# Kernel tuning notes

Hardware: AMD Instinct MI355X
Metric: run time of the kernel (lower is better)

Reference implementation:

```python
import jax, jax.numpy as jnp
import numpy as np

B, N = 32, 512            # batch, max nodes per graph
F_DIM, M_DIM = 1024, 256  # node feature dim, first hidden dim
N_SEM = 8                 # number of semantic-class experts
XYZ, DIM_E = 3, 8
OUT_SIZE = 2 * XYZ + DIM_E  # 14 (default reg branch)
EPS = 1e-8                # padding value used by out_seq_to_batch


def setup_inputs() -> dict:
    key = jax.random.key(0)
    ks = jax.random.split(key, 12)
    def w(k, shape, fan_in):
        return jax.random.normal(k, shape, jnp.float32) / np.float32(np.sqrt(fan_in))
    return {
        "nodes": jax.random.normal(ks[0], (B, N, F_DIM), jnp.float32),
        "sem": jax.random.randint(ks[1], (B, N), 0, N_SEM, jnp.int32),
        "lengths": jax.random.randint(ks[2], (B,), 64, N + 1, jnp.int32),
        # y expert MLPs (4 layers), stacked over experts
        "W1": w(ks[3], (N_SEM, F_DIM, M_DIM), F_DIM), "b1": jnp.zeros((N_SEM, M_DIM), jnp.float32),
        "W2": w(ks[4], (N_SEM, M_DIM, 64), M_DIM),   "b2": jnp.zeros((N_SEM, 64), jnp.float32),
        "W3": w(ks[5], (N_SEM, 64, 32), 64),         "b3": jnp.zeros((N_SEM, 32), jnp.float32),
        "W4": w(ks[6], (N_SEM, 32, OUT_SIZE), 32),   "b4": jnp.zeros((N_SEM, OUT_SIZE), jnp.float32),
        # rot expert MLPs (2 layers), stacked over experts
        "R1": w(ks[7], (N_SEM, F_DIM, M_DIM), F_DIM), "rb1": jnp.zeros((N_SEM, M_DIM), jnp.float32),
        "R2": w(ks[8], (N_SEM, M_DIM, XYZ), M_DIM),   "rb2": jnp.zeros((N_SEM, XYZ), jnp.float32),
    }


def _prim_mlps(nodes, sem, lengths, W1, b1, W2, b2, W3, b3, W4, b4, R1, rb1, R2, rb2):
    Bn, Nn, Fd = nodes.shape
    x = nodes.reshape(-1, Fd)                       # [T, F], T = B*N tokens
    semf = sem.reshape(-1)                          # [T] expert id per token
    # dense dispatch: run every expert on all tokens, then select per token
    h1 = jax.nn.relu(jnp.einsum('tf,efm->etm', x, W1) + b1[:, None, :])   # [E,T,M]
    h2 = jax.nn.relu(jnp.einsum('etm,emh->eth', h1, W2) + b2[:, None, :]) # [E,T,64]
    h3 = jax.nn.relu(jnp.einsum('eth,ehg->etg', h2, W3) + b3[:, None, :]) # [E,T,32]
    y_all = jnp.einsum('etg,ego->eto', h3, W4) + b4[:, None, :]           # [E,T,OUT]
    r1 = jax.nn.relu(jnp.einsum('tf,efm->etm', x, R1) + rb1[:, None, :])  # [E,T,M]
    rot_all = jnp.einsum('etm,emo->eto', r1, R2) + rb2[:, None, :]        # [E,T,XYZ]
    t = jnp.arange(x.shape[0])
    y = y_all[semf, t]                              # [T, OUT]
    rot = rot_all[semf, t]                          # [T, XYZ]
    out = jnp.concatenate([y, rot], axis=-1).reshape(Bn, Nn, -1)
    # positions beyond each graph's length are filled with eps (out_seq_to_batch)
    mask = (jnp.arange(Nn)[None, :] < lengths[:, None])[:, :, None]
    return jnp.where(mask, out, jnp.float32(EPS))


def reference(nodes, sem, lengths, W1, b1, W2, b2, W3, b3, W4, b4, R1, rb1, R2, rb2):
    return _prim_mlps(nodes, sem, lengths, W1, b1, W2, b2, W3, b3, W4, b4,
                      R1, rb1, R2, rb2)
```

## Files before the change

kernel.cpp:

```cpp
#include <hip/hip_runtime.h>
#include <stdint.h>

#define T_TOK 16384
#define NE 8
#define EPSV 1e-8f
#define MAXC128 136
#define MAXC64  264

#define WS_PERM   0
#define WS_PART   65536
#define WS_OFFS   67584
#define WS_WT     131072
#define WS_H1     (WS_WT + 8*512*1024*2)
#define WS_W2T    (WS_H1 + 16448*512*2)
#define WS_W3T    (WS_W2T + 8*64*256*2)
#define WS_W4T    (WS_W3T + 8*32*64*2)
#define WS_R2T    (WS_W4T + 8*16*32*2)

typedef __attribute__((ext_vector_type(8))) short bf16x8;
typedef __attribute__((ext_vector_type(4))) float f32x4;

__device__ __forceinline__ unsigned short f2bf(float f) {
    unsigned u = __float_as_uint(f);
    u += 0x7fffu + ((u >> 16) & 1u);
    return (unsigned short)(u >> 16);
}

__device__ __forceinline__ void gl_lds16(const void* g, void* l) {
    __builtin_amdgcn_global_load_lds(
        (const __attribute__((address_space(1))) void*)g,
        (__attribute__((address_space(3))) void*)l,
        16, 0, 0);
}

__device__ __forceinline__ bool chunk_lookup(const int* __restrict__ offs, int c, int csize,
                                             int& e, int& base, int& len) {
    int acc = 0;
#pragma unroll
    for (int i = 0; i < NE; i++) {
        int s = offs[i], t = offs[i + 1];
        int cc = (t - s + csize - 1) / csize;
        if (c < acc + cc) {
            e = i;
            base = s + (c - acc) * csize;
            len = (t - base < csize) ? (t - base) : csize;
            return true;
        }
        acc += cc;
    }
    return false;
}

__global__ __launch_bounds__(256) void k_prep1(const float* __restrict__ W1,
                                               const float* __restrict__ R1,
                                               const float* __restrict__ W2,
                                               const float* __restrict__ W3,
                                               const float* __restrict__ W4,
                                               const float* __restrict__ R2,
                                               const int* __restrict__ sem,
                                               unsigned short* __restrict__ wt,
                                               unsigned short* __restrict__ w2t,
                                               unsigned short* __restrict__ w3t,
                                               unsigned short* __restrict__ w4t,
                                               unsigned short* __restrict__ r2t,
                                               int* __restrict__ ws_i) {
    __shared__ float tile[64][65];
    int id = blockIdx.x, tid = threadIdx.x;
    if (id >= 1024) {
        __shared__ int cnt[NE];
        int hb = id - 1024, lane = tid & 63;
        if (tid < NE) cnt[tid] = 0;
        __syncthreads();
        int s = sem[hb * 256 + tid];
#pragma unroll
        for (int e = 0; e < NE; e++) {
            unsigned long long m = __ballot(s == e);
            if (lane == e) atomicAdd(&cnt[e], (int)__popcll(m));
        }
        __syncthreads();
        if (tid < NE) ws_i[(WS_PART >> 2) + hb * NE + tid] = cnt[tid];
        return;
    }
    int e = id >> 7, rem = id & 127;
    int ny = rem >> 4, kx = rem & 15;
    int k0 = kx * 64, n0 = ny * 64;
    const float* src = (n0 < 256) ? (W1 + (size_t)e * 1024 * 256 + n0)
                                  : (R1 + (size_t)e * 1024 * 256 + (n0 - 256));
    int rr = tid >> 4;
    int cg = (tid & 15) * 4;
#pragma unroll
    for (int p = 0; p < 4; p++) {
        int kk = p * 16 + rr;
        float4 v = *(const float4*)(src + (size_t)(k0 + kk) * 256 + cg);
        tile[kk][cg] = v.x; tile[kk][cg + 1] = v.y; tile[kk][cg + 2] = v.z; tile[kk][cg + 3] = v.w;
    }
    __syncthreads();
    int nn = tid >> 3;
    int k8 = tid & 7;
#pragma unroll
    for (int p = 0; p < 2; p++) {
        int n = p * 32 + nn;
        unsigned w[4];
#pragma unroll
        for (int j = 0; j < 4; j++) {
            float f0 = tile[k8 * 8 + 2 * j][n];
            float f1 = tile[k8 * 8 + 2 * j + 1][n];
            w[j] = (unsigned)f2bf(f0) | ((unsigned)f2bf(f1) << 16);
        }
        *(uint4*)(wt + (size_t)(e * 512 + n0 + n) * 1024 + k0 + k8 * 8) =
            make_uint4(w[0], w[1], w[2], w[3]);
    }
    if (ny == 0) {
        int x = kx;
        for (int j = tid; j < 1024; j += 256) {
            int idx = x * 1024 + j; int k = idx & 255, n = idx >> 8;
            w2t[(size_t)(e * 64 + n) * 256 + k] = f2bf(W2[(size_t)e * 16384 + k * 64 + n]);
        }
        if (tid < 128) {
            int idx = x * 128 + tid; int k = idx & 63, n = idx >> 6;
            w3t[(size_t)(e * 32 + n) * 64 + k] = f2bf(W3[(size_t)e * 2048 + k * 32 + n]);
        }
        if (tid < 32) {
            int idx = x * 32 + tid; int k = idx & 31, n = idx >> 5;
            w4t[(size_t)(e * 16 + n) * 32 + k] = (n < 14) ? f2bf(W4[(size_t)e * 448 + k * 14 + n])
                                                          : (unsigned short)0;
        }
        {
            int idx = x * 256 + tid; int k = idx & 255, n = idx >> 8;
            r2t[(size_t)(e * 16 + n) * 256 + k] = (n < 3) ? f2bf(R2[(size_t)e * 768 + k * 3 + n])
                                                          : (unsigned short)0;
        }
    }
}

__global__ __launch_bounds__(256) void k_scatter(const int* __restrict__ sem, int* __restrict__ ws_i) {
    __shared__ int parts[64 * NE];
    __shared__ int tot[NE], preb[NE], ebase[NE + 1];
    __shared__ int cur[NE];
    int b = blockIdx.x, tid = threadIdx.x, lane = tid & 63;
    parts[tid] = ws_i[(WS_PART >> 2) + tid];
    parts[256 + tid] = ws_i[(WS_PART >> 2) + 256 + tid];
    __syncthreads();
    if (tid < NE) {
        int t = 0, p = 0;
        for (int bb = 0; bb < 64; bb++) {
            int v = parts[bb * NE + tid];
            t += v;
            if (bb < b) p += v;
        }
        tot[tid] = t; preb[tid] = p;
    }
    __syncthreads();
    if (tid == 0) {
        int base = 0;
        for (int e = 0; e < NE; e++) { ebase[e] = base; base += tot[e]; }
        ebase[NE] = base;
        if (b == 0)
            for (int e = 0; e <= NE; e++) ws_i[(WS_OFFS >> 2) + e] = ebase[e];
    }
    __syncthreads();
    if (tid < NE) cur[tid] = ebase[tid] + preb[tid];
    __syncthreads();
    int i = b * 256 + tid;
    int s = sem[i];
    int* perm = ws_i + (WS_PERM >> 2);
#pragma unroll
    for (int e = 0; e < NE; e++) {
        unsigned long long m = __ballot(s == e);
        if (s == e) {
            int leader = (int)__builtin_ctzll(m);
            int rank = (int)__popcll(m & ((1ull << lane) - 1ull));
            int bpos = 0;
            if (lane == leader) bpos = atomicAdd(&cur[e], (int)__popcll(m));
            bpos = __shfl(bpos, leader, 64);
            perm[bpos + rank] = i;
        }
    }
}

__global__ __launch_bounds__(256) void k_gemm(const float* __restrict__ nodes,
                                              const unsigned short* __restrict__ wt,
                                              const float* __restrict__ b1,
                                              const float* __restrict__ rb1,
                                              const int* __restrict__ ws_i,
                                              unsigned short* __restrict__ h1) {
    __shared__ __align__(16) short As[128 * 64];
    __shared__ __align__(16) short Bs[128 * 64];
    int e, base, len;
    if (!chunk_lookup(ws_i + (WS_OFFS >> 2), blockIdx.x, 128, e, base, len)) return;
    int n0 = blockIdx.y * 128;
    int tid = threadIdx.x;
    int wave = tid >> 6, lane = tid & 63;
    int quad = lane >> 4, lr = lane & 15;
    int wm = (wave & 1) * 64, wn = (wave >> 1) * 64;
    const int* perm = ws_i + (WS_PERM >> 2);

    f32x4 acc[4][4];
#pragma unroll
    for (int i = 0; i < 4; i++)
#pragma unroll
        for (int j = 0; j < 4; j++) acc[i][j] = (f32x4){0.f, 0.f, 0.f, 0.f};

    const unsigned short* Bg = wt + (size_t)(e * 512 + n0) * 1024;

    int cs = (tid & 7) ^ ((tid >> 3) & 7);
    const float* srcA[4];
    const unsigned short* srcB[4];
    int dstA[4], dstB[4];
#pragma unroll
    for (int i = 0; i < 4; i++) {
        int R = i * 32 + (tid >> 3);
        int row = base + R; if (row > T_TOK - 1) row = T_TOK - 1;
        srcA[i] = nodes + (size_t)perm[row] * 1024 + cs * 8;
        dstA[i] = (i * 256 + tid) * 8;
        int s = i * 256 + wave * 64 + lane;
        int r = s >> 3, cb = (s & 7) ^ (r & 7);
        srcB[i] = Bg + (size_t)r * 1024 + cb * 8;
        dstB[i] = (i * 256 + wave * 64) * 8;
    }

    for (int kb = 0; kb < 16; kb++) {
        __syncthreads();
#pragma unroll
        for (int i = 0; i < 4; i++)
            gl_lds16(srcB[i] + kb * 64, Bs + dstB[i]);
#pragma unroll
        for (int i = 0; i < 4; i++) {
            const float4* p = (const float4*)(srcA[i] + kb * 64);
            float4 a = p[0], b = p[1];
            unsigned r0 = (unsigned)f2bf(a.x) | ((unsigned)f2bf(a.y) << 16);
            unsigned r1 = (unsigned)f2bf(a.z) | ((unsigned)f2bf(a.w) << 16);
            unsigned r2 = (unsigned)f2bf(b.x) | ((unsigned)f2bf(b.y) << 16);
            unsigned r3 = (unsigned)f2bf(b.z) | ((unsigned)f2bf(b.w) << 16);
            *(uint4*)(As + dstA[i]) = make_uint4(r0, r1, r2, r3);
        }
        __syncthreads();

        bf16x8 af[2][4], bfr[2][4];
#pragma unroll
        for (int im = 0; im < 4; im++) {
            int r = wm + im * 16 + lr;
#pragma unroll
            for (int kh = 0; kh < 2; kh++) {
                int q = kh * 4 + quad;
                af[kh][im] = *(const bf16x8*)(As + (r * 8 + (q ^ (r & 7))) * 8);
            }
        }
#pragma unroll
        for (int in = 0; in < 4; in++) {
            int r = wn + in * 16 + lr;
#pragma unroll
            for (int kh = 0; kh < 2; kh++) {
                int q = kh * 4 + quad;
                bfr[kh][in] = *(const bf16x8*)(Bs + (r * 8 + (q ^ (r & 7))) * 8);
            }
        }
#pragma unroll
        for (int kh = 0; kh < 2; kh++)
#pragma unroll
            for (int im = 0; im < 4; im++)
#pragma unroll
                for (int in = 0; in < 4; in++)
                    acc[im][in] = __builtin_amdgcn_mfma_f32_16x16x32_bf16(af[kh][im], bfr[kh][in], acc[im][in], 0, 0, 0);
    }

#pragma unroll
    for (int in = 0; in < 4; in++) {
        int gcol = n0 + wn + in * 16 + lr;
        float bias = (gcol < 256) ? b1[e * 256 + gcol] : rb1[e * 256 + gcol - 256];
#pragma unroll
        for (int im = 0; im < 4; im++) {
#pragma unroll
            for (int v = 0; v < 4; v++) {
                int r = wm + im * 16 + quad * 4 + v;
                if (r < len) {
                    float val = fmaxf(acc[im][in][v] + bias, 0.f);
                    h1[(size_t)(base + r) * 512 + gcol] = f2bf(val);
                }
            }
        }
    }
}

__global__ __launch_bounds__(256) void k_tail(const unsigned short* __restrict__ h1,
                                              const int* __restrict__ ws_i,
                                              const unsigned short* __restrict__ w2t,
                                              const unsigned short* __restrict__ w3t,
                                              const unsigned short* __restrict__ w4t,
                                              const unsigned short* __restrict__ r2t,
                                              const float* __restrict__ b2,
                                              const float* __restrict__ b3,
                                              const float* __restrict__ b4,
                                              const float* __restrict__ rb2,
                                              const int* __restrict__ lengths,
                                              float* __restrict__ out) {
    __shared__ __align__(16) unsigned short h2s[4][16][64];
    __shared__ __align__(16) unsigned short h3s[4][16][32];

    int e, base, len;
    if (!chunk_lookup(ws_i + (WS_OFFS >> 2), blockIdx.x, 64, e, base, len)) return;
    int tid = threadIdx.x, wave = tid >> 6, lane = tid & 63;
    int quad = lane >> 4, lr = lane & 15;
    int m0 = wave * 16;

    const unsigned short* Ap = h1 + (size_t)(base + m0) * 512;

    f32x4 acc2[4];
#pragma unroll
    for (int t = 0; t < 4; t++) {
        float bb = b2[e * 64 + t * 16 + lr];
        acc2[t] = (f32x4){bb, bb, bb, bb};
    }
    f32x4 accr;
    { float bb = (lr < 3) ? rb2[e * 3 + lr] : 0.f; accr = (f32x4){bb, bb, bb, bb}; }

    const unsigned short* W2e = w2t + (size_t)e * 64 * 256;
    const unsigned short* R2e = r2t + (size_t)e * 16 * 256;
#pragma unroll
    for (int kk = 0; kk < 8; kk++) {
        int k0 = kk * 32;
        bf16x8 a = *(const bf16x8*)(Ap + lr * 512 + k0 + quad * 8);
#pragma unroll
        for (int t = 0; t < 4; t++) {
            bf16x8 b = *(const bf16x8*)(W2e + (t * 16 + lr) * 256 + k0 + quad * 8);
            acc2[t] = __builtin_amdgcn_mfma_f32_16x16x32_bf16(a, b, acc2[t], 0, 0, 0);
        }
        bf16x8 ar = *(const bf16x8*)(Ap + lr * 512 + 256 + k0 + quad * 8);
        bf16x8 br = *(const bf16x8*)(R2e + lr * 256 + k0 + quad * 8);
        accr = __builtin_amdgcn_mfma_f32_16x16x32_bf16(ar, br, accr, 0, 0, 0);
    }
#pragma unroll
    for (int t = 0; t < 4; t++)
#pragma unroll
        for (int v = 0; v < 4; v++)
            h2s[wave][quad * 4 + v][t * 16 + lr] = f2bf(fmaxf(acc2[t][v], 0.f));

    f32x4 acc3[2];
#pragma unroll
    for (int t = 0; t < 2; t++) {
        float bb = b3[e * 32 + t * 16 + lr];
        acc3[t] = (f32x4){bb, bb, bb, bb};
    }
    const unsigned short* W3e = w3t + (size_t)e * 32 * 64;
#pragma unroll
    for (int kk = 0; kk < 2; kk++) {
        int k0 = kk * 32;
        bf16x8 a = *(const bf16x8*)(&h2s[wave][lr][k0 + quad * 8]);
#pragma unroll
        for (int t = 0; t < 2; t++) {
            bf16x8 b = *(const bf16x8*)(W3e + (t * 16 + lr) * 64 + k0 + quad * 8);
            acc3[t] = __builtin_amdgcn_mfma_f32_16x16x32_bf16(a, b, acc3[t], 0, 0, 0);
        }
    }
#pragma unroll
    for (int t = 0; t < 2; t++)
#pragma unroll
        for (int v = 0; v < 4; v++)
            h3s[wave][quad * 4 + v][t * 16 + lr] = f2bf(fmaxf(acc3[t][v], 0.f));

    f32x4 acc4;
    { float bb = (lr < 14) ? b4[e * 14 + lr] : 0.f; acc4 = (f32x4){bb, bb, bb, bb}; }
    {
        bf16x8 a = *(const bf16x8*)(&h3s[wave][lr][quad * 8]);
        bf16x8 b = *(const bf16x8*)(w4t + ((size_t)e * 16 + lr) * 32 + quad * 8);
        acc4 = __builtin_amdgcn_mfma_f32_16x16x32_bf16(a, b, acc4, 0, 0, 0);
    }

    const int* perm = ws_i + (WS_PERM >> 2);
#pragma unroll
    for (int v = 0; v < 4; v++) {
        int t = m0 + quad * 4 + v;
        if (t < len) {
            int token = perm[base + t];
            int bi = token >> 9, ni = token & 511;
            int valid = ni < lengths[bi];
            if (lr < 14) out[(size_t)token * 17 + lr] = valid ? acc4[v] : EPSV;
            if (lr < 3)  out[(size_t)token * 17 + 14 + lr] = valid ? accr[v] : EPSV;
        }
    }
}

extern "C" void kernel_launch(void* const* d_in, const int* in_sizes, int n_in,
                              void* d_out, int out_size, void* d_ws, size_t ws_size,
                              hipStream_t stream) {
    (void)in_sizes; (void)n_in; (void)out_size; (void)ws_size;
    const float* nodes   = (const float*)d_in[0];
    const int*   sem     = (const int*)d_in[1];
    const int*   lengths = (const int*)d_in[2];
    const float* W1 = (const float*)d_in[3];
    const float* b1 = (const float*)d_in[4];
    const float* W2 = (const float*)d_in[5];
    const float* b2 = (const float*)d_in[6];
    const float* W3 = (const float*)d_in[7];
    const float* b3 = (const float*)d_in[8];
    const float* W4 = (const float*)d_in[9];
    const float* b4 = (const float*)d_in[10];
    const float* R1  = (const float*)d_in[11];
    const float* rb1 = (const float*)d_in[12];
    const float* R2  = (const float*)d_in[13];
    const float* rb2 = (const float*)d_in[14];
    float* out = (float*)d_out;

    char* ws = (char*)d_ws;
    int* ws_i = (int*)ws;
    unsigned short* wt  = (unsigned short*)(ws + WS_WT);
    unsigned short* h1  = (unsigned short*)(ws + WS_H1);
    unsigned short* w2t = (unsigned short*)(ws + WS_W2T);
    unsigned short* w3t = (unsigned short*)(ws + WS_W3T);
    unsigned short* w4t = (unsigned short*)(ws + WS_W4T);
    unsigned short* r2t = (unsigned short*)(ws + WS_R2T);

    hipLaunchKernelGGL(k_prep1, dim3(1088), dim3(256), 0, stream,
                       W1, R1, W2, W3, W4, R2, sem, wt, w2t, w3t, w4t, r2t, ws_i);
    hipLaunchKernelGGL(k_scatter, dim3(64), dim3(256), 0, stream, sem, ws_i);
    hipLaunchKernelGGL(k_gemm, dim3(MAXC128, 4), dim3(256), 0, stream,
                       nodes, (const unsigned short*)wt, b1, rb1, (const int*)ws_i, h1);
    hipLaunchKernelGGL(k_tail, dim3(MAXC64), dim3(256), 0, stream,
                       (const unsigned short*)h1, (const int*)ws_i,
                       (const unsigned short*)w2t, (const unsigned short*)w3t,
                       (const unsigned short*)w4t, (const unsigned short*)r2t,
                       b2, b3, b4, rb2, lengths, out);
}
```

Before: 213.4 us.

## Pre-gather and convert node features to bf16 sorted buffer before GEMM

The scatter kernel now also converts node rows to bf16 and writes them in expert-sorted order into a new workspace buffer, using a deterministic per-wave prefix instead of shared atomics. The grid grows to 512 blocks, each copying 32 rows. The first-layer GEMM then loads A tiles through the direct global-to-LDS path with no per-tile fp32 conversion. Previously the GEMM re-read and re-converted each fp32 row once for every one of its 4 N-blocks. The cost is an extra bf16 write and read of the whole activation matrix.

```diff
diff --git a/kernel.cpp b/kernel.cpp
--- a/kernel.cpp
+++ b/kernel.cpp
@@ -10,7 +10,8 @@
 #define WS_PERM   0
 #define WS_PART   65536
 #define WS_OFFS   67584
-#define WS_WT     131072
+#define WS_XS     131072
+#define WS_WT     (WS_XS + 16512*1024*2)
 #define WS_H1     (WS_WT + 8*512*1024*2)
 #define WS_W2T    (WS_H1 + 16448*512*2)
 #define WS_W3T    (WS_W2T + 8*64*256*2)
@@ -133,11 +134,16 @@
     }
 }
 
-__global__ __launch_bounds__(256) void k_scatter(const int* __restrict__ sem, int* __restrict__ ws_i) {
-    __shared__ int parts[64 * NE];
+__global__ __launch_bounds__(256) void k_scatter(const int* __restrict__ sem,
+                                                 const float* __restrict__ nodes,
+                                                 int* __restrict__ ws_i,
+                                                 unsigned short* __restrict__ xs) {
+    __shared__ int parts[512];
     __shared__ int tot[NE], preb[NE], ebase[NE + 1];
-    __shared__ int cur[NE];
-    int b = blockIdx.x, tid = threadIdx.x, lane = tid & 63;
+    __shared__ int wcnt[4][NE];
+    __shared__ int destS[256];
+    int b = blockIdx.x, g = b >> 3, j = b & 7;
+    int tid = threadIdx.x, wave = tid >> 6, lane = tid & 63;
     parts[tid] = ws_i[(WS_PART >> 2) + tid];
     parts[256 + tid] = ws_i[(WS_PART >> 2) + 256 + tid];
     __syncthreads();
@@ -146,7 +152,7 @@
         for (int bb = 0; bb < 64; bb++) {
             int v = parts[bb * NE + tid];
             t += v;
-            if (bb < b) p += v;
+            if (bb < g) p += v;
         }
         tot[tid] = t; preb[tid] = p;
     }
@@ -158,27 +164,36 @@
         if (b == 0)
             for (int e = 0; e <= NE; e++) ws_i[(WS_OFFS >> 2) + e] = ebase[e];
     }
-    __syncthreads();
-    if (tid < NE) cur[tid] = ebase[tid] + preb[tid];
-    __syncthreads();
-    int i = b * 256 + tid;
+    int i = g * 256 + tid;
     int s = sem[i];
-    int* perm = ws_i + (WS_PERM >> 2);
+    int rank = 0;
 #pragma unroll
     for (int e = 0; e < NE; e++) {
         unsigned long long m = __ballot(s == e);
-        if (s == e) {
-            int leader = (int)__builtin_ctzll(m);
-            int rank = (int)__popcll(m & ((1ull << lane) - 1ull));
-            int bpos = 0;
-            if (lane == leader) bpos = atomicAdd(&cur[e], (int)__popcll(m));
-            bpos = __shfl(bpos, leader, 64);
-            perm[bpos + rank] = i;
-        }
-    }
-}
-
-__global__ __launch_bounds__(256) void k_gemm(const float* __restrict__ nodes,
+        if (s == e) rank = (int)__popcll(m & ((1ull << lane) - 1ull));
+        if (lane == e) wcnt[wave][e] = (int)__popcll(m);
+    }
+    __syncthreads();
+    int wpre = 0;
+#pragma unroll
+    for (int w = 0; w < 4; w++)
+        if (w < wave) wpre += wcnt[w][s];
+    int dest = ebase[s] + preb[s] + wpre + rank;
+    destS[tid] = dest;
+    if (j == 0) ws_i[(WS_PERM >> 2) + dest] = i;
+    __syncthreads();
+#pragma unroll 4
+    for (int r = j * 32; r < j * 32 + 32; r++) {
+        int tok = g * 256 + r;
+        int d = destS[r];
+        float4 v = *(const float4*)(nodes + (size_t)tok * 1024 + tid * 4);
+        unsigned p0 = (unsigned)f2bf(v.x) | ((unsigned)f2bf(v.y) << 16);
+        unsigned p1 = (unsigned)f2bf(v.z) | ((unsigned)f2bf(v.w) << 16);
+        *(uint2*)(xs + (size_t)d * 1024 + tid * 4) = make_uint2(p0, p1);
+    }
+}
+
+__global__ __launch_bounds__(256) void k_gemm(const unsigned short* __restrict__ xs,
                                               const unsigned short* __restrict__ wt,
                                               const float* __restrict__ b1,
                                               const float* __restrict__ rb1,
@@ -193,7 +208,6 @@
     int wave = tid >> 6, lane = tid & 63;
     int quad = lane >> 4, lr = lane & 15;
     int wm = (wave & 1) * 64, wn = (wave >> 1) * 64;
-    const int* perm = ws_i + (WS_PERM >> 2);
 
     f32x4 acc[4][4];
 #pragma unroll
@@ -201,38 +215,27 @@
 #pragma unroll
         for (int j = 0; j < 4; j++) acc[i][j] = (f32x4){0.f, 0.f, 0.f, 0.f};
 
+    const unsigned short* Ag = xs + (size_t)base * 1024;
     const unsigned short* Bg = wt + (size_t)(e * 512 + n0) * 1024;
 
-    int cs = (tid & 7) ^ ((tid >> 3) & 7);
-    const float* srcA[4];
+    const unsigned short* srcA[4];
     const unsigned short* srcB[4];
-    int dstA[4], dstB[4];
+    int dst[4];
 #pragma unroll
     for (int i = 0; i < 4; i++) {
-        int R = i * 32 + (tid >> 3);
-        int row = base + R; if (row > T_TOK - 1) row = T_TOK - 1;
-        srcA[i] = nodes + (size_t)perm[row] * 1024 + cs * 8;
-        dstA[i] = (i * 256 + tid) * 8;
         int s = i * 256 + wave * 64 + lane;
-        int r = s >> 3, cb = (s & 7) ^ (r & 7);
-        srcB[i] = Bg + (size_t)r * 1024 + cb * 8;
-        dstB[i] = (i * 256 + wave * 64) * 8;
+        int r = s >> 3, cs = (s & 7) ^ (r & 7);
+        srcA[i] = Ag + (size_t)r * 1024 + cs * 8;
+        srcB[i] = Bg + (size_t)r * 1024 + cs * 8;
+        dst[i] = (i * 256 + wave * 64) * 8;
     }
 
     for (int kb = 0; kb < 16; kb++) {
         __syncthreads();
 #pragma unroll
-        for (int i = 0; i < 4; i++)
-            gl_lds16(srcB[i] + kb * 64, Bs + dstB[i]);
-#pragma unroll
         for (int i = 0; i < 4; i++) {
-            const float4* p = (const float4*)(srcA[i] + kb * 64);
-            float4 a = p[0], b = p[1];
-            unsigned r0 = (unsigned)f2bf(a.x) | ((unsigned)f2bf(a.y) << 16);
-            unsigned r1 = (unsigned)f2bf(a.z) | ((unsigned)f2bf(a.w) << 16);
-            unsigned r2 = (unsigned)f2bf(b.x) | ((unsigned)f2bf(b.y) << 16);
-            unsigned r3 = (unsigned)f2bf(b.z) | ((unsigned)f2bf(b.w) << 16);
-            *(uint4*)(As + dstA[i]) = make_uint4(r0, r1, r2, r3);
+            gl_lds16(srcA[i] + kb * 64, As + dst[i]);
+            gl_lds16(srcB[i] + kb * 64, Bs + dst[i]);
         }
         __syncthreads();
 
@@ -403,6 +406,7 @@
 
     char* ws = (char*)d_ws;
     int* ws_i = (int*)ws;
+    unsigned short* xs  = (unsigned short*)(ws + WS_XS);
     unsigned short* wt  = (unsigned short*)(ws + WS_WT);
     unsigned short* h1  = (unsigned short*)(ws + WS_H1);
     unsigned short* w2t = (unsigned short*)(ws + WS_W2T);
@@ -412,9 +416,10 @@
 
     hipLaunchKernelGGL(k_prep1, dim3(1088), dim3(256), 0, stream,
                        W1, R1, W2, W3, W4, R2, sem, wt, w2t, w3t, w4t, r2t, ws_i);
-    hipLaunchKernelGGL(k_scatter, dim3(64), dim3(256), 0, stream, sem, ws_i);
+    hipLaunchKernelGGL(k_scatter, dim3(512), dim3(256), 0, stream, sem, nodes, ws_i, xs);
     hipLaunchKernelGGL(k_gemm, dim3(MAXC128, 4), dim3(256), 0, stream,
-                       nodes, (const unsigned short*)wt, b1, rb1, (const int*)ws_i, h1);
+                       (const unsigned short*)xs, (const unsigned short*)wt, b1, rb1,
+                       (const int*)ws_i, h1);
     hipLaunchKernelGGL(k_tail, dim3(MAXC64), dim3(256), 0, stream,
                        (const unsigned short*)h1, (const int*)ws_i,
                        (const unsigned short*)w2t, (const unsigned short*)w3t,
```

Measured after the change: 198.7 us. 1.07x faster.
